# Optimization experiments

Hardware: AMD Instinct MI355X
Metric: run time of the kernel (lower is better)

Reference implementation:

```python
import jax, jax.numpy as jnp
import numpy as np

IMG_H, IMG_W = 256, 704  # full image shape (img_metas['img_shape'])
EPS = 1e-5
B, N_CAM, D_REF, C_CH = 1, 6, 1, 256
HF, WF = 32, 88
DD = 64
BEV_H = BEV_W = 128
Q = BEV_H * BEV_W


def inverse_sigmoid(x, eps=1e-5):
    x = jnp.clip(x, 0.0, 1.0)
    return jnp.log(jnp.clip(x, eps) / jnp.clip(1.0 - x, eps))


def grid_sample_2d(feat, grid):
    # feat [N,C,H,W], grid [N,Hg,Wg,2] (x,y in [-1,1]); bilinear, zeros padding, align_corners=False
    Nn, C, H, W = feat.shape
    x = (grid[..., 0] + 1.0) * 0.5 * W - 0.5
    y = (grid[..., 1] + 1.0) * 0.5 * H - 0.5
    x0 = jnp.floor(x)
    y0 = jnp.floor(y)
    wx = x - x0
    wy = y - y0
    x0 = x0.astype(jnp.int32)
    y0 = y0.astype(jnp.int32)

    def gather(ix, iy):
        valid = (ix >= 0) & (ix < W) & (iy >= 0) & (iy < H)
        ixc = jnp.clip(ix, 0, W - 1)
        iyc = jnp.clip(iy, 0, H - 1)
        v = jax.vmap(lambda f, jx, jy: f[:, jy, jx])(feat, ixc, iyc)  # [N,C,Hg,Wg]
        return v * valid[:, None].astype(feat.dtype)

    return (gather(x0, y0) * ((1 - wx) * (1 - wy))[:, None]
            + gather(x0 + 1, y0) * (wx * (1 - wy))[:, None]
            + gather(x0, y0 + 1) * ((1 - wx) * wy)[:, None]
            + gather(x0 + 1, y0 + 1) * (wx * wy)[:, None])


def grid_sample_3d(vol, grid):
    # vol [N,C,D,H,W], grid [N,Dg,Hg,Wg,3] (x,y,z); trilinear, zeros padding, align_corners=False
    Nn, C, D, H, W = vol.shape
    x = (grid[..., 0] + 1.0) * 0.5 * W - 0.5
    y = (grid[..., 1] + 1.0) * 0.5 * H - 0.5
    z = (grid[..., 2] + 1.0) * 0.5 * D - 0.5
    x0 = jnp.floor(x); y0 = jnp.floor(y); z0 = jnp.floor(z)
    wx = x - x0; wy = y - y0; wz = z - z0
    x0 = x0.astype(jnp.int32); y0 = y0.astype(jnp.int32); z0 = z0.astype(jnp.int32)

    def gather(ix, iy, iz):
        valid = (ix >= 0) & (ix < W) & (iy >= 0) & (iy < H) & (iz >= 0) & (iz < D)
        ixc = jnp.clip(ix, 0, W - 1)
        iyc = jnp.clip(iy, 0, H - 1)
        izc = jnp.clip(iz, 0, D - 1)
        v = jax.vmap(lambda f, jx, jy, jz: f[:, jz, jy, jx])(vol, ixc, iyc, izc)
        return v * valid[:, None].astype(vol.dtype)

    return (gather(x0, y0, z0) * ((1 - wx) * (1 - wy) * (1 - wz))[:, None]
            + gather(x0 + 1, y0, z0) * (wx * (1 - wy) * (1 - wz))[:, None]
            + gather(x0, y0 + 1, z0) * ((1 - wx) * wy * (1 - wz))[:, None]
            + gather(x0 + 1, y0 + 1, z0) * (wx * wy * (1 - wz))[:, None]
            + gather(x0, y0, z0 + 1) * ((1 - wx) * (1 - wy) * wz)[:, None]
            + gather(x0 + 1, y0, z0 + 1) * (wx * (1 - wy) * wz)[:, None]
            + gather(x0, y0 + 1, z0 + 1) * ((1 - wx) * wy * wz)[:, None]
            + gather(x0 + 1, y0 + 1, z0 + 1) * (wx * wy * wz)[:, None])


def setup_inputs() -> dict:
    key = jax.random.key(0)
    ks = jax.random.split(key, 12)
    feat = jax.random.normal(ks[0], (B * N_CAM, C_CH, HF, WF), jnp.float32)
    bev_queries = jax.random.normal(ks[1], (B, Q, C_CH), jnp.float32)
    bev_pos = jax.random.normal(ks[2], (B, Q, C_CH), jnp.float32)
    reference_points = jax.random.uniform(ks[3], (B, D_REF, Q, 3), jnp.float32)
    pc_range = jnp.array([-51.2, -51.2, -5.0, 51.2, 51.2, 3.0], jnp.float32)
    # semi-realistic lidar->image projection matrices: intrinsics * axis-swap * yaw per camera
    f, cx, cy = 500.0, IMG_W / 2.0, IMG_H / 2.0
    K = np.array([[f, 0, cx, 0], [0, f, cy, 0], [0, 0, 1, 0], [0, 0, 0, 1]], np.float32)
    A = np.array([[0, -1, 0, 0], [0, 0, -1, 0], [1, 0, 0, 0], [0, 0, 0, 1]], np.float32)
    mats = []
    for i in range(N_CAM):
        th = 2.0 * np.pi * i / N_CAM
        c, s = np.cos(th), np.sin(th)
        R = np.array([[c, s, 0, 0], [-s, c, 0, 0], [0, 0, 1, 0], [0, 0, 0, 1]], np.float32)
        mats.append(K @ A @ R)
    lidar_to_img = jnp.asarray(np.stack(mats))[None]  # [1,N,4,4]
    depth_prob = jax.random.uniform(ks[4], (B * N_CAM, DD, HF, WF), jnp.float32)
    sc = 0.02
    return {
        'feat': feat, 'bev_queries': bev_queries, 'bev_pos': bev_pos,
        'reference_points': reference_points, 'pc_range': pc_range,
        'lidar_to_img': lidar_to_img, 'depth_prob': depth_prob,
        'w_pos': jax.random.normal(ks[5], (C_CH, 1), jnp.float32) * sc,
        'b_pos': jnp.zeros((1,), jnp.float32),
        'w_img': jax.random.normal(ks[6], (C_CH, N_CAM * 2), jnp.float32) * sc,
        'b_img': jnp.zeros((N_CAM * 2,), jnp.float32),
        'w_att': jax.random.normal(ks[7], (C_CH, N_CAM), jnp.float32) * sc,
        'b_att': jnp.zeros((N_CAM,), jnp.float32),
        'conv_w': jax.random.normal(ks[8], (C_CH, C_CH, 3, 3), jnp.float32) * sc,
        'conv_b': jnp.zeros((C_CH,), jnp.float32),
        'bn_gamma': jnp.ones((C_CH,), jnp.float32),
        'bn_beta': jnp.zeros((C_CH,), jnp.float32),
        'bn_mean': jnp.zeros((C_CH,), jnp.float32),
        'bn_var': jnp.ones((C_CH,), jnp.float32),
        'se_w': jax.random.normal(ks[9], (C_CH, C_CH), jnp.float32) * sc,
        'se_b': jnp.zeros((C_CH,), jnp.float32),
        'cbam_w': jax.random.normal(ks[10], (1, 2, 7, 7), jnp.float32) * 0.05,
        'cbam_b': jnp.zeros((1,), jnp.float32),
        'bev_h': BEV_H, 'bev_w': BEV_W,
    }


def reference(feat, bev_queries, bev_pos, reference_points, pc_range, lidar_to_img, depth_prob,
              w_pos, b_pos, w_img, b_img, w_att, b_att, conv_w, conv_b,
              bn_gamma, bn_beta, bn_mean, bn_var, se_w, se_b, cbam_w, cbam_b, bev_h, bev_w):
    Bq, Qn = bev_queries.shape[:2]
    D = reference_points.shape[1]
    N = lidar_to_img.shape[1]
    BN, C, Hf, Wf = feat.shape
    q = bev_queries + bev_pos
    pos_offset = q @ w_pos + b_pos  # [B,Q,1] (only_use_height)
    z = jax.nn.sigmoid(inverse_sigmoid(reference_points[..., 2:3]) + pos_offset[:, None])
    rp = jnp.concatenate([reference_points[..., :2], z], axis=-1)  # [B,D,Q,3]
    attn = (q @ w_att + b_att).reshape(Bq, 1, Qn, N, 1)
    img_off = q @ w_img + b_img  # [B,Q,2N]
    # unnormalize to lidar coords; apply_3d_transformation == identity (no aug)
    pts = rp * (pc_range[3:] - pc_range[:3]) + pc_range[:3]
    pts4 = jnp.concatenate([pts, jnp.ones_like(pts[..., :1])], axis=-1)  # [B,D,Q,4]
    cam = jnp.einsum('bnij,bdqj->dbnqi', lidar_to_img, pts4)  # [D,B,N,Q,4]
    ref_depth = cam[..., 2:3]
    mask = ref_depth > EPS
    xy = cam[..., :2] / jnp.maximum(cam[..., 2:3], EPS)
    xy = xy / jnp.array([IMG_W, IMG_H], dtype=xy.dtype)
    xy = (xy - 0.5) * 2.0
    mask = mask & (xy[..., 0:1] > -1.0) & (xy[..., 0:1] < 1.0) & (xy[..., 1:2] > -1.0) & (xy[..., 1:2] < 1.0)
    Dd = depth_prob.shape[1]
    ref_depth = (ref_depth / Dd - 0.5) * 2.0
    mask = mask & (ref_depth > -1.0) & (ref_depth < 1.0)
    bev_mask = jnp.transpose(mask, (1, 4, 3, 2, 0)).astype(feat.dtype)  # [B,1,Q,N,D]
    off = img_off.reshape(Bq, Qn, N, 2).transpose(0, 2, 1, 3)[None] / jnp.array([Wf, Hf], dtype=feat.dtype)
    xy = xy + off  # [D,B,N,Q,2]
    grid = xy.transpose(1, 2, 3, 0, 4).reshape(BN, Qn, D, 2)
    sampled = grid_sample_2d(feat, grid).reshape(Bq, N, C, Qn, D).transpose(0, 2, 3, 1, 4)  # [B,C,Q,N,D]
    grid3 = jnp.concatenate([xy, ref_depth], axis=-1).transpose(1, 2, 3, 0, 4).reshape(BN, 1, Qn, D, 3)
    dp = grid_sample_3d(depth_prob[:, None], grid3).reshape(Bq, N, 1, Qn, D).transpose(0, 2, 3, 1, 4)
    bev_mask = jnp.nan_to_num(dp) * bev_mask
    w = jax.nn.sigmoid(attn) * jnp.nan_to_num(bev_mask)
    agg = (jnp.nan_to_num(sampled) * w)[..., 0].sum(-1)  # [B,C,Q] (D==1)
    x = agg.reshape(Bq, C, bev_h, bev_w)
    dn = ('NCHW', 'OIHW', 'NCHW')
    x = jax.lax.conv_general_dilated(x, conv_w, (1, 1), ((1, 1), (1, 1)), dimension_numbers=dn) + conv_b[None, :, None, None]
    x = (x - bn_mean[None, :, None, None]) * (bn_gamma / jnp.sqrt(bn_var + 1e-5))[None, :, None, None] + bn_beta[None, :, None, None]
    x = jax.nn.relu(x)
    s = x.mean(axis=(2, 3))  # SE: global avg pool + 1x1 conv + sigmoid
    x = x * jax.nn.sigmoid(s @ se_w.T + se_b)[:, :, None, None]
    a = jnp.concatenate([x.max(axis=1, keepdims=True), x.mean(axis=1, keepdims=True)], axis=1)  # CBAM spatial
    a = jax.lax.conv_general_dilated(a, cbam_w, (1, 1), ((3, 3), (3, 3)), dimension_numbers=dn) + cbam_b[None, :, None, None]
    x = x * jax.nn.sigmoid(a)
    out = x.reshape(Bq, C, bev_h * bev_w).transpose(0, 2, 1)
    return out, rp
```

## Files before the change

kernel.cpp:

```cpp
#include <hip/hip_runtime.h>
#include <math.h>

#define QN   16384
#define CCH  256
#define NCAM 6
#define HFD  32
#define WFD  88
#define DDD  64
#define BEVH 128
#define BEVW 128
#define IMGW 704.0f
#define IMGH 256.0f
#define EPSV 1e-5f

typedef __attribute__((ext_vector_type(8))) short bf8_t;
typedef __attribute__((ext_vector_type(8))) unsigned short us8;
typedef __attribute__((ext_vector_type(4))) unsigned short us4;
typedef __attribute__((ext_vector_type(4))) float f4_t;

__device__ __forceinline__ float sigmoidf_(float x){ return 1.0f/(1.0f+__expf(-x)); }

__device__ __forceinline__ unsigned short f2bf(float f){
    unsigned int b = __float_as_uint(f);
    b += 0x7FFFu + ((b >> 16) & 1u);
    return (unsigned short)(b >> 16);
}
__device__ __forceinline__ float bf2f(unsigned short u){
    return __uint_as_float(((unsigned int)u) << 16);
}

__global__ __launch_bounds__(256) void k_prep(const float* __restrict__ feat, unsigned short* __restrict__ feat_tH,
                                              const float* __restrict__ cw, unsigned short* __restrict__ wtH,
                                              const float* __restrict__ se_w, float* __restrict__ se_wT,
                                              float* __restrict__ ssum){
    int b = blockIdx.x;
    if (b < 4224){
        __shared__ float tile[32][33];
        int n   = b / 704;
        int rem = b - n*704;
        int cb  = (rem / 88) * 32;
        int pb  = (rem % 88) * 32;
        int tx = threadIdx.x & 31, ty = threadIdx.x >> 5;
        for (int r = ty; r < 32; r += 8)
            tile[r][tx] = feat[(size_t)(n*256 + cb + r)*2816 + pb + tx];
        __syncthreads();
        for (int r = ty; r < 32; r += 8)
            feat_tH[(size_t)(n*2816 + pb + r)*256 + cb + tx] = f2bf(tile[tx][r]);
    } else if (b < 6528){
        int b2 = b - 4224;
        if (b2 == 0) ssum[threadIdx.x] = 0.f;
        int idx = b2*256 + threadIdx.x;
        int ci = idx & 255;
        int co = (idx >> 8) & 255;
        int kk = idx >> 16;
        int kh = kk/3, kw = kk - kh*3;
        int chunk = ci >> 6, ciin = ci & 63;
        size_t dst = ((((size_t)(kh*4 + chunk)*3 + kw)*256 + co) << 6) + ciin;
        wtH[dst] = f2bf(cw[(size_t)(co*256 + ci)*9 + kk]);
    } else {
        __shared__ float tile[32][33];
        int tb = b - 6528;
        int rb_ = (tb >> 3) * 32;
        int cb_ = (tb & 7) * 32;
        int tx = threadIdx.x & 31, ty = threadIdx.x >> 5;
        for (int r = ty; r < 32; r += 8)
            tile[r][tx] = se_w[(size_t)(rb_ + r)*256 + cb_ + tx];
        __syncthreads();
        for (int r = ty; r < 32; r += 8)
            se_wT[(size_t)(cb_ + r)*256 + rb_ + tx] = tile[tx][r];
    }
}

__global__ __launch_bounds__(256) void k_proj(
    const float* __restrict__ bq, const float* __restrict__ bpos,
    const float* __restrict__ refp,
    const float* __restrict__ w_pos, const float* __restrict__ b_pos,
    const float* __restrict__ w_img, const float* __restrict__ w_att,
    float* __restrict__ Sg, float* __restrict__ out_rp)
{
    __shared__ float wlf[19][260];
    __shared__ unsigned short Aq[64][264];
    __shared__ float sl[64][20];
    int tid = threadIdx.x;
    int lane = tid & 63, wid = tid >> 6;
    int l15 = lane & 15, quad = lane >> 4;
    int q0 = blockIdx.x * 64;

    wlf[0][tid] = w_pos[tid];
    #pragma unroll
    for (int r = 0; r < 6; r++){
        int idx = r*256 + tid;
        int c = idx / 6, j = idx - 6*c;
        wlf[1 + j][c] = w_att[idx];
    }
    #pragma unroll
    for (int r = 0; r < 12; r++){
        int idx = r*256 + tid;
        int c = idx / 12, j = idx - 12*c;
        wlf[7 + j][c] = w_img[idx];
    }
    #pragma unroll
    for (int r = 0; r < 16; r++){
        int row = r*4 + wid;
        int cc  = lane * 4;
        float4 a = *(const float4*)(bq   + (size_t)(q0+row)*CCH + cc);
        float4 b = *(const float4*)(bpos + (size_t)(q0+row)*CCH + cc);
        us4 o;
        o.x = f2bf(a.x+b.x); o.y = f2bf(a.y+b.y); o.z = f2bf(a.z+b.z); o.w = f2bf(a.w+b.w);
        *(us4*)&Aq[row][cc] = o;
    }
    __syncthreads();

    f4_t acc0 = (f4_t){0.f,0.f,0.f,0.f};
    f4_t acc1 = (f4_t){0.f,0.f,0.f,0.f};
    #pragma unroll
    for (int kc = 0; kc < 8; kc++){
        bf8_t af = *(bf8_t*)&Aq[wid*16 + l15][kc*32 + quad*8];
        bf8_t b0, b1;
        {
            const float* wr = &wlf[l15][kc*32 + quad*8];
            float4 w0 = *(const float4*)wr;
            float4 w1 = *(const float4*)(wr + 4);
            b0[0]=(short)f2bf(w0.x); b0[1]=(short)f2bf(w0.y); b0[2]=(short)f2bf(w0.z); b0[3]=(short)f2bf(w0.w);
            b0[4]=(short)f2bf(w1.x); b0[5]=(short)f2bf(w1.y); b0[6]=(short)f2bf(w1.z); b0[7]=(short)f2bf(w1.w);
        }
        if (l15 < 3){
            const float* wr = &wlf[16 + l15][kc*32 + quad*8];
            float4 w0 = *(const float4*)wr;
            float4 w1 = *(const float4*)(wr + 4);
            b1[0]=(short)f2bf(w0.x); b1[1]=(short)f2bf(w0.y); b1[2]=(short)f2bf(w0.z); b1[3]=(short)f2bf(w0.w);
            b1[4]=(short)f2bf(w1.x); b1[5]=(short)f2bf(w1.y); b1[6]=(short)f2bf(w1.z); b1[7]=(short)f2bf(w1.w);
        } else {
            b1 = (bf8_t){0,0,0,0,0,0,0,0};
        }
        acc0 = __builtin_amdgcn_mfma_f32_16x16x32_bf16(af, b0, acc0, 0, 0, 0);
        acc1 = __builtin_amdgcn_mfma_f32_16x16x32_bf16(af, b1, acc1, 0, 0, 0);
    }
    #pragma unroll
    for (int r = 0; r < 4; r++){
        int qq = wid*16 + quad*4 + r;
        sl[qq][l15] = acc0[r];
        if (l15 < 3) sl[qq][16 + l15] = acc1[r];
    }
    __syncthreads();

    if (tid < 64){
        int q = q0 + tid;
        float pos_off = sl[tid][0] + b_pos[0];
        float rx = refp[q*3+0], ry = refp[q*3+1], rz = refp[q*3+2];
        float zc_ = fminf(fmaxf(rz, 0.f), 1.f);
        float inv = logf(fmaxf(zc_, EPSV) / fmaxf(1.f - zc_, EPSV));
        float znew = sigmoidf_(inv + pos_off);
        out_rp[q*3+0] = rx; out_rp[q*3+1] = ry; out_rp[q*3+2] = znew;
        sl[tid][19] = znew;
    }
    __syncthreads();

    for (int i = tid; i < 64*20; i += 256)
        Sg[(size_t)q0*20 + i] = ((const float*)sl)[i];
}

__global__ __launch_bounds__(256) void k_geomagg(
    const float* __restrict__ refp, const float* __restrict__ pcr,
    const float* __restrict__ l2i, const float* __restrict__ dpr,
    const float* __restrict__ b_img, const float* __restrict__ b_att,
    const float* __restrict__ Sg, const unsigned short* __restrict__ feat_tH,
    unsigned short* __restrict__ aggH)
{
    __shared__ float sgl[8][20];
    __shared__ int   so_l[192];
    __shared__ float sw_l[192];
    int q0 = blockIdx.x * 8;
    int tid = threadIdx.x;
    int wid = tid >> 6, lane = tid & 63;

    if (tid < 160) ((float*)sgl)[tid] = Sg[(size_t)q0*20 + tid];
    __syncthreads();

    {
        int sub = lane >> 5;
        int n   = lane & 31;
        if (n < NCAM){
            int ql = wid*2 + sub;
            int q  = q0 + ql;
            float att  = sgl[ql][1+n] + b_att[n];
            float offx = (sgl[ql][7+2*n] + b_img[2*n])   / (float)WFD;
            float offy = (sgl[ql][8+2*n] + b_img[2*n+1]) / (float)HFD;
            float znew = sgl[ql][19];
            float rx = refp[q*3+0], ry = refp[q*3+1];
            float lo0=pcr[0], lo1=pcr[1], lo2=pcr[2];
            float hi0=pcr[3], hi1=pcr[4], hi2=pcr[5];
            float px = rx*(hi0-lo0)+lo0, py = ry*(hi1-lo1)+lo1, pz = znew*(hi2-lo2)+lo2;
            const float* M = l2i + n*16;
            float cx = M[0]*px + M[1]*py + M[2]*pz  + M[3];
            float cy = M[4]*px + M[5]*py + M[6]*pz  + M[7];
            float cz = M[8]*px + M[9]*py + M[10]*pz + M[11];
            bool m = cz > EPSV;
            float zdiv = fmaxf(cz, EPSV);
            float u = (cx/zdiv)/IMGW; u = (u - 0.5f)*2.f;
            float v = (cy/zdiv)/IMGH; v = (v - 0.5f)*2.f;
            m = m && (u > -1.f) && (u < 1.f) && (v > -1.f) && (v < 1.f);
            float rdn = (cz/(float)DDD - 0.5f)*2.f;
            m = m && (rdn > -1.f) && (rdn < 1.f);

            int base = ql*24 + n*4;
            float wq = 0.f, xs = 0.f, ys = 0.f;
            if (m){
                float u2 = u + offx, v2 = v + offy;
                xs = (u2 + 1.f)*0.5f*WFD - 0.5f;
                ys = (v2 + 1.f)*0.5f*HFD - 0.5f;
                float zs = (rdn + 1.f)*0.5f*DDD - 0.5f;
                float fx = floorf(xs), fy = floorf(ys), fz = floorf(zs);
                int x0=(int)fx, y0=(int)fy, z0=(int)fz;
                float wx = xs-fx, wy = ys-fy, wz = zs-fz;
                float dp = 0.f;
                const float* vol = dpr + (size_t)n*DDD*HFD*WFD;
                #pragma unroll
                for (int dz=0; dz<2; dz++)
                #pragma unroll
                for (int dy=0; dy<2; dy++)
                #pragma unroll
                for (int dx=0; dx<2; dx++){
                    int ix=x0+dx, iy=y0+dy, iz=z0+dz;
                    if (ix>=0 && ix<WFD && iy>=0 && iy<HFD && iz>=0 && iz<DDD){
                        float ww = (dx?wx:1.f-wx)*(dy?wy:1.f-wy)*(dz?wz:1.f-wz);
                        dp += ww * vol[(size_t)(iz*HFD+iy)*WFD + ix];
                    }
                }
                wq = sigmoidf_(att) * dp;
            }
            if (m && wq != 0.f){
                float fx = floorf(xs), fy = floorf(ys);
                int x0=(int)fx, y0=(int)fy;
                float wx = xs-fx, wy = ys-fy;
                float cwv[4] = {(1.f-wx)*(1.f-wy), wx*(1.f-wy), (1.f-wx)*wy, wx*wy};
                int xi[4] = {x0, x0+1, x0, x0+1};
                int yi[4] = {y0, y0, y0+1, y0+1};
                #pragma unroll
                for (int k=0;k<4;k++){
                    bool ok = (xi[k]>=0 && xi[k]<WFD && yi[k]>=0 && yi[k]<HFD);
                    so_l[base+k] = ok ? ((n*HFD + yi[k])*WFD + xi[k]) : 0;
                    sw_l[base+k] = ok ? wq*cwv[k] : 0.f;
                }
            } else {
                #pragma unroll
                for (int k=0;k<4;k++){ so_l[base+k] = 0; sw_l[base+k] = 0.f; }
            }
        }
    }
    __syncthreads();

    {
        int half = lane >> 5, li = lane & 31;
        int c8 = li * 8;
        int ql = wid*2 + half;
        float a[8] = {0.f,0.f,0.f,0.f,0.f,0.f,0.f,0.f};
        #pragma unroll
        for (int k=0;k<24;k++){
            float w = sw_l[ql*24+k];
            us8 v = *(const us8*)(feat_tH + (size_t)so_l[ql*24+k]*CCH + c8);
            #pragma unroll
            for (int j=0;j<8;j++) a[j] += w * bf2f((unsigned short)v[j]);
        }
        us8 o;
        #pragma unroll
        for (int j=0;j<8;j++) o[j] = f2bf(a[j]);
        *(us8*)(aggH + (size_t)(q0+ql)*CCH + c8) = o;
    }
}

__global__ __launch_bounds__(256, 2) void k_conv2(const unsigned short* __restrict__ aggH,
    const unsigned short* __restrict__ wtH, const float* __restrict__ conv_b,
    const float* __restrict__ bn_g, const float* __restrict__ bn_b,
    const float* __restrict__ bn_m, const float* __restrict__ bn_v,
    float* __restrict__ xN, float* __restrict__ ssum)
{
    __shared__ unsigned short Al[130][72];
    __shared__ unsigned short Bl[3][128][72];
    __shared__ float sacc[128];

    int h   = blockIdx.x;
    int co0 = blockIdx.y * 128;
    int tid  = threadIdx.x;
    int lane = tid & 63, wid = tid >> 6;
    int m_q = (wid & 1) * 64;
    int n_q = (wid >> 1) * 64;
    int l15 = lane & 15, quad = lane >> 4;

    f4_t acc[4][4];
    #pragma unroll
    for (int i=0;i<4;i++)
    #pragma unroll
    for (int j=0;j<4;j++) acc[i][j] = (f4_t){0.f,0.f,0.f,0.f};

    int arow = tid >> 1;
    int aseg = (tid & 1) * 32;

    if (tid < 16){
        int r = (tid >> 3) ? 129 : 0;
        int sg = (tid & 7) * 8;
        *(us8*)&Al[r][sg] = (us8){0,0,0,0,0,0,0,0};
    }
    if (tid < 128) sacc[tid] = 0.f;

    us8 ra[4], rb[3][4];
    const us8 z8 = (us8){0,0,0,0,0,0,0,0};

    #define LOADSTAGE(s) { \
        int kh_ = (s) >> 2; \
        int ph_ = h + kh_ - 1; \
        if (ph_ >= 0 && ph_ < BEVH){ \
            const unsigned short* ap_ = aggH + ((size_t)(ph_*BEVW + arow)*CCH + (((s) & 3) << 6) + aseg); \
            ra[0] = *(const us8*)ap_;        ra[1] = *(const us8*)(ap_ + 8); \
            ra[2] = *(const us8*)(ap_ + 16); ra[3] = *(const us8*)(ap_ + 24); \
        } else { ra[0]=z8; ra[1]=z8; ra[2]=z8; ra[3]=z8; } \
        const unsigned short* bp_ = wtH + (size_t)(s)*49152 + (size_t)co0*64; \
        _Pragma("unroll") \
        for (int kw_=0; kw_<3; kw_++){ \
            _Pragma("unroll") \
            for (int j_=0; j_<4; j_++) \
                rb[kw_][j_] = *(const us8*)(bp_ + kw_*16384 + (j_*256 + tid)*8); \
        } \
    }

    LOADSTAGE(0);
    for (int s=0; s<12; s++){
        __syncthreads();
        *(us8*)&Al[arow+1][aseg]      = ra[0];
        *(us8*)&Al[arow+1][aseg+8]    = ra[1];
        *(us8*)&Al[arow+1][aseg+16]   = ra[2];
        *(us8*)&Al[arow+1][aseg+24]   = ra[3];
        {
            int bco = tid >> 3;
            int ciin = (tid & 7) * 8;
            #pragma unroll
            for (int kw_=0; kw_<3; kw_++){
                #pragma unroll
                for (int j_=0; j_<4; j_++)
                    *(us8*)&Bl[kw_][j_*32 + bco][ciin] = rb[kw_][j_];
            }
        }
        __syncthreads();
        if (s < 11) LOADSTAGE(s+1);
        #pragma unroll
        for (int ks=0; ks<2; ks++){
            #pragma unroll
            for (int kw=0; kw<3; kw++){
                bf8_t af[4], bfr[4];
                #pragma unroll
                for (int i=0;i<4;i++) af[i]  = *(bf8_t*)&Al[m_q + i*16 + l15 + kw][ks*32 + quad*8];
                #pragma unroll
                for (int j=0;j<4;j++) bfr[j] = *(bf8_t*)&Bl[kw][n_q + j*16 + l15][ks*32 + quad*8];
                #pragma unroll
                for (int i=0;i<4;i++)
                #pragma unroll
                for (int j=0;j<4;j++)
                    acc[i][j] = __builtin_amdgcn_mfma_f32_16x16x32_bf16(af[i], bfr[j], acc[i][j], 0, 0, 0);
            }
        }
    }
    #undef LOADSTAGE

    #pragma unroll
    for (int j=0;j<4;j++){
        int col = n_q + j*16 + l15;
        int co = co0 + col;
        float sc = bn_g[co] * rsqrtf(bn_v[co] + 1e-5f);
        float sh = bn_b[co] - bn_m[co]*sc;
        float cb = conv_b[co];
        float part = 0.f;
        #pragma unroll
        for (int i=0;i<4;i++){
            #pragma unroll
            for (int r=0;r<4;r++){
                int m = m_q + i*16 + quad*4 + r;
                int p = h*BEVW + m;
                float y = fmaxf((acc[i][j][r] + cb)*sc + sh, 0.f);
                xN[(size_t)p*CCH + co] = y;
                part += y;
            }
        }
        atomicAdd(&sacc[col], part);
    }
    __syncthreads();
    if (tid < 128) atomicAdd(&ssum[co0 + tid], sacc[tid]);
}

__global__ __launch_bounds__(256) void k_maps2(const float* __restrict__ xN,
    const float* __restrict__ ssum, const float* __restrict__ se_wT, const float* __restrict__ se_b,
    float* __restrict__ scale_g, float* __restrict__ amax, float* __restrict__ amean)
{
    __shared__ float smv[256];
    __shared__ float scl[256];
    int t = threadIdx.x;
    smv[t] = ssum[t] * (1.f/16384.f);
    __syncthreads();
    float a0=0.f, a1=0.f, a2=0.f, a3=0.f;
    for (int k=0; k<256; k+=4){
        a0 += smv[k]   * se_wT[(size_t)(k  )*256 + t];
        a1 += smv[k+1] * se_wT[(size_t)(k+1)*256 + t];
        a2 += smv[k+2] * se_wT[(size_t)(k+2)*256 + t];
        a3 += smv[k+3] * se_wT[(size_t)(k+3)*256 + t];
    }
    float sv = sigmoidf_(se_b[t] + ((a0+a1)+(a2+a3)));
    scl[t] = sv;
    if (blockIdx.x == 0) scale_g[t] = sv;
    __syncthreads();

    int wid = t >> 6, lane = t & 63;
    int p0 = blockIdx.x * 64;
    float4 sc = *(const float4*)&scl[lane*4];
    for (int i=0; i<16; i++){
        int p = p0 + i*4 + wid;
        float4 v = *(const float4*)&xN[(size_t)p*CCH + lane*4];
        float a = v.x*sc.x, b = v.y*sc.y, c = v.z*sc.z, d = v.w*sc.w;
        float mx = fmaxf(fmaxf(a,b), fmaxf(c,d));
        float sm = a+b+c+d;
        #pragma unroll
        for (int off=1; off<64; off<<=1){
            mx = fmaxf(mx, __shfl_xor(mx, off, 64));
            sm += __shfl_xor(sm, off, 64);
        }
        if (lane == 0){ amax[p] = mx; amean[p] = sm*(1.f/256.f); }
    }
}

__global__ __launch_bounds__(256) void k_final2(const float* __restrict__ xN,
    const float* __restrict__ scale_g, const float* __restrict__ amax, const float* __restrict__ amean,
    const float* __restrict__ cw, const float* __restrict__ cb, float* __restrict__ out)
{
    __shared__ float am2[7][128];
    __shared__ float av2[7][128];
    __shared__ float wcb[98];
    __shared__ float scl[256];
    __shared__ float amap_l[64];

    int b = blockIdx.x;
    int h  = b >> 1;
    int w0 = (b & 1) * 64;
    int t = threadIdx.x;

    scl[t] = scale_g[t];
    if (t < 98) wcb[t] = cw[t];
    for (int idx = t; idx < 896; idx += 256){
        int r = idx >> 7, c = idx & 127;
        int ph = h + r - 3;
        bool ok = (ph >= 0 && ph < BEVH);
        am2[r][c] = ok ? amax[ph*BEVW + c] : 0.f;
        av2[r][c] = ok ? amean[ph*BEVW + c] : 0.f;
    }
    __syncthreads();

    if (t < 64){
        int px = w0 + t;
        float acc = cb[0];
        #pragma unroll
        for (int kh=0; kh<7; kh++){
            #pragma unroll
            for (int kw=0; kw<7; kw++){
                int pw = px + kw - 3;
                if (pw >= 0 && pw < BEVW)
                    acc += am2[kh][pw]*wcb[kh*7+kw] + av2[kh][pw]*wcb[49 + kh*7+kw];
            }
        }
        amap_l[t] = sigmoidf_(acc);
    }
    __syncthreads();

    int lane = t & 63, sub = t >> 6;
    int c4 = lane * 4;
    float4 sc = *(const float4*)&scl[c4];
    for (int i=0; i<16; i++){
        int pxl = sub*16 + i;
        int p = h*BEVW + w0 + pxl;
        float am = amap_l[pxl];
        float4 v = *(const float4*)&xN[(size_t)p*CCH + c4];
        float4 o;
        o.x = v.x*sc.x*am; o.y = v.y*sc.y*am; o.z = v.z*sc.z*am; o.w = v.w*sc.w*am;
        *(float4*)&out[(size_t)p*CCH + c4] = o;
    }
}

extern "C" void kernel_launch(void* const* d_in, const int* in_sizes, int n_in,
                              void* d_out, int out_size, void* d_ws, size_t ws_size,
                              hipStream_t stream) {
    const float* feat   = (const float*)d_in[0];
    const float* bq     = (const float*)d_in[1];
    const float* bpos   = (const float*)d_in[2];
    const float* refp   = (const float*)d_in[3];
    const float* pcr    = (const float*)d_in[4];
    const float* l2i    = (const float*)d_in[5];
    const float* dpr    = (const float*)d_in[6];
    const float* w_pos  = (const float*)d_in[7];
    const float* b_pos  = (const float*)d_in[8];
    const float* w_img  = (const float*)d_in[9];
    const float* b_img  = (const float*)d_in[10];
    const float* w_att  = (const float*)d_in[11];
    const float* b_att  = (const float*)d_in[12];
    const float* conv_w = (const float*)d_in[13];
    const float* conv_b = (const float*)d_in[14];
    const float* bn_g   = (const float*)d_in[15];
    const float* bn_b   = (const float*)d_in[16];
    const float* bn_m   = (const float*)d_in[17];
    const float* bn_v   = (const float*)d_in[18];
    const float* se_w   = (const float*)d_in[19];
    const float* se_b   = (const float*)d_in[20];
    const float* cbw    = (const float*)d_in[21];
    const float* cbb    = (const float*)d_in[22];
    float* out = (float*)d_out;

    float* ws = (float*)d_ws;
    size_t o = 0;
    unsigned short* feat_tH = (unsigned short*)(ws + o); o += (size_t)6*2816*128;
    unsigned short* wtH  = (unsigned short*)(ws + o); o += (size_t)9*256*128;
    unsigned short* aggH = (unsigned short*)(ws + o); o += (size_t)QN*128;
    float* xN      = ws + o;  o += (size_t)QN*256;
    float* se_wT   = ws + o;  o += (size_t)256*256;
    float* Sg      = ws + o;  o += (size_t)QN*20;
    float* ssum    = ws + o;  o += 256;
    float* scale_g = ws + o;  o += 256;
    float* amax    = ws + o;  o += QN;
    float* amean   = ws + o;  o += QN;

    k_prep<<<6592, 256, 0, stream>>>(feat, feat_tH, conv_w, wtH, se_w, se_wT, ssum);
    k_proj<<<256, 256, 0, stream>>>(bq, bpos, refp, w_pos, b_pos, w_img, w_att,
                                    Sg, out + (size_t)QN*256);
    k_geomagg<<<2048, 256, 0, stream>>>(refp, pcr, l2i, dpr, b_img, b_att,
                                        Sg, feat_tH, aggH);
    k_conv2<<<dim3(128,2), 256, 0, stream>>>(aggH, wtH, conv_b, bn_g, bn_b, bn_m, bn_v, xN, ssum);
    k_maps2<<<256, 256, 0, stream>>>(xN, ssum, se_wT, se_b, scale_g, amax, amean);
    k_final2<<<256, 256, 0, stream>>>(xN, scale_g, amax, amean, cbw, cbb, out);
}
```

Measured before the change: 221.2 us.

## Split conv K dimension across two blocks and add separate activation reduce kernel

The 3x3 conv kernel now splits its 12 K-stages between two z-blocks, doubling the grid from 256 to 512 blocks so more CUs are occupied. Each block writes raw fp32 partial sums to its own buffer. A new k_act kernel adds the two partials, applies bias, batchnorm and ReLU, and accumulates the SE channel sums. The LDS row padding also changes from 72 to 76 to alter the bank mapping. The cost is two extra 16 MB fp32 buffers, one written and later read, plus an additional kernel launch.

After: 247.8 us. +12.0%, slower.

```diff
diff --git a/kernel.cpp b/kernel.cpp
--- a/kernel.cpp
+++ b/kernel.cpp
@@ -270,17 +270,15 @@
 }
 
 __global__ __launch_bounds__(256, 2) void k_conv2(const unsigned short* __restrict__ aggH,
-    const unsigned short* __restrict__ wtH, const float* __restrict__ conv_b,
-    const float* __restrict__ bn_g, const float* __restrict__ bn_b,
-    const float* __restrict__ bn_m, const float* __restrict__ bn_v,
-    float* __restrict__ xN, float* __restrict__ ssum)
+    const unsigned short* __restrict__ wtH,
+    float* __restrict__ xNa, float* __restrict__ xNb)
 {
-    __shared__ unsigned short Al[130][72];
-    __shared__ unsigned short Bl[3][128][72];
-    __shared__ float sacc[128];
+    __shared__ unsigned short Al[130][76];
+    __shared__ unsigned short Bl[3][128][76];
 
     int h   = blockIdx.x;
     int co0 = blockIdx.y * 128;
+    int z   = blockIdx.z;
     int tid  = threadIdx.x;
     int lane = tid & 63, wid = tid >> 6;
     int m_q = (wid & 1) * 64;
@@ -301,20 +299,20 @@
         int sg = (tid & 7) * 8;
         *(us8*)&Al[r][sg] = (us8){0,0,0,0,0,0,0,0};
     }
-    if (tid < 128) sacc[tid] = 0.f;
 
     us8 ra[4], rb[3][4];
     const us8 z8 = (us8){0,0,0,0,0,0,0,0};
 
-    #define LOADSTAGE(s) { \
-        int kh_ = (s) >> 2; \
+    #define SFULL(sp) ((((sp) >> 1) << 2) + (z << 1) + ((sp) & 1))
+    #define LOADSTAGE(sf) { \
+        int kh_ = (sf) >> 2; \
         int ph_ = h + kh_ - 1; \
         if (ph_ >= 0 && ph_ < BEVH){ \
-            const unsigned short* ap_ = aggH + ((size_t)(ph_*BEVW + arow)*CCH + (((s) & 3) << 6) + aseg); \
+            const unsigned short* ap_ = aggH + ((size_t)(ph_*BEVW + arow)*CCH + (((sf) & 3) << 6) + aseg); \
             ra[0] = *(const us8*)ap_;        ra[1] = *(const us8*)(ap_ + 8); \
             ra[2] = *(const us8*)(ap_ + 16); ra[3] = *(const us8*)(ap_ + 24); \
         } else { ra[0]=z8; ra[1]=z8; ra[2]=z8; ra[3]=z8; } \
-        const unsigned short* bp_ = wtH + (size_t)(s)*49152 + (size_t)co0*64; \
+        const unsigned short* bp_ = wtH + (size_t)(sf)*49152 + (size_t)co0*64; \
         _Pragma("unroll") \
         for (int kw_=0; kw_<3; kw_++){ \
             _Pragma("unroll") \
@@ -323,8 +321,8 @@
         } \
     }
 
-    LOADSTAGE(0);
-    for (int s=0; s<12; s++){
+    LOADSTAGE(SFULL(0));
+    for (int sp=0; sp<6; sp++){
         __syncthreads();
         *(us8*)&Al[arow+1][aseg]      = ra[0];
         *(us8*)&Al[arow+1][aseg+8]    = ra[1];
@@ -341,7 +339,7 @@
             }
         }
         __syncthreads();
-        if (s < 11) LOADSTAGE(s+1);
+        if (sp < 5) LOADSTAGE(SFULL(sp+1));
         #pragma unroll
         for (int ks=0; ks<2; ks++){
             #pragma unroll
@@ -360,30 +358,68 @@
         }
     }
     #undef LOADSTAGE
-
+    #undef SFULL
+
+    float* __restrict__ xO = z ? xNb : xNa;
     #pragma unroll
     for (int j=0;j<4;j++){
-        int col = n_q + j*16 + l15;
-        int co = co0 + col;
-        float sc = bn_g[co] * rsqrtf(bn_v[co] + 1e-5f);
-        float sh = bn_b[co] - bn_m[co]*sc;
-        float cb = conv_b[co];
-        float part = 0.f;
+        int co = co0 + n_q + j*16 + l15;
         #pragma unroll
         for (int i=0;i<4;i++){
             #pragma unroll
             for (int r=0;r<4;r++){
                 int m = m_q + i*16 + quad*4 + r;
-                int p = h*BEVW + m;
-                float y = fmaxf((acc[i][j][r] + cb)*sc + sh, 0.f);
-                xN[(size_t)p*CCH + co] = y;
-                part += y;
+                xO[(size_t)(h*BEVW + m)*CCH + co] = acc[i][j][r];
             }
         }
-        atomicAdd(&sacc[col], part);
-    }
-    __syncthreads();
-    if (tid < 128) atomicAdd(&ssum[co0 + tid], sacc[tid]);
+    }
+}
+
+__global__ __launch_bounds__(256) void k_act(const float* __restrict__ xNa, const float* __restrict__ xNb,
+    const float* __restrict__ conv_b, const float* __restrict__ bn_g, const float* __restrict__ bn_b,
+    const float* __restrict__ bn_m, const float* __restrict__ bn_v,
+    float* __restrict__ xN, float* __restrict__ ssum)
+{
+    __shared__ float red[4][256];
+    int t = threadIdx.x, lane = t & 63, wid = t >> 6;
+    int c4 = lane * 4;
+    float4 g  = *(const float4*)&bn_g[c4];
+    float4 vv = *(const float4*)&bn_v[c4];
+    float4 mm = *(const float4*)&bn_m[c4];
+    float4 bb = *(const float4*)&bn_b[c4];
+    float4 cb = *(const float4*)&conv_b[c4];
+    float4 sc, sh;
+    sc.x = g.x*rsqrtf(vv.x+1e-5f); sc.y = g.y*rsqrtf(vv.y+1e-5f);
+    sc.z = g.z*rsqrtf(vv.z+1e-5f); sc.w = g.w*rsqrtf(vv.w+1e-5f);
+    sh.x = bb.x - mm.x*sc.x; sh.y = bb.y - mm.y*sc.y;
+    sh.z = bb.z - mm.z*sc.z; sh.w = bb.w - mm.w*sc.w;
+
+    float4 sum = {0.f,0.f,0.f,0.f};
+    int p0 = blockIdx.x * 64;
+    for (int i=0;i<16;i++){
+        int p = p0 + i*4 + wid;
+        float4 a = *(const float4*)&xNa[(size_t)p*CCH + c4];
+        float4 b = *(const float4*)&xNb[(size_t)p*CCH + c4];
+        float4 y;
+        y.x = fmaxf((a.x+b.x+cb.x)*sc.x+sh.x, 0.f);
+        y.y = fmaxf((a.y+b.y+cb.y)*sc.y+sh.y, 0.f);
+        y.z = fmaxf((a.z+b.z+cb.z)*sc.z+sh.z, 0.f);
+        y.w = fmaxf((a.w+b.w+cb.w)*sc.w+sh.w, 0.f);
+        *(float4*)&xN[(size_t)p*CCH + c4] = y;
+        sum.x += y.x; sum.y += y.y; sum.z += y.z; sum.w += y.w;
+    }
+    *(float4*)&red[wid][c4] = sum;
+    __syncthreads();
+    if (wid == 0){
+        float4 s0 = *(const float4*)&red[0][c4];
+        float4 s1 = *(const float4*)&red[1][c4];
+        float4 s2 = *(const float4*)&red[2][c4];
+        float4 s3 = *(const float4*)&red[3][c4];
+        atomicAdd(&ssum[c4+0], (s0.x+s1.x)+(s2.x+s3.x));
+        atomicAdd(&ssum[c4+1], (s0.y+s1.y)+(s2.y+s3.y));
+        atomicAdd(&ssum[c4+2], (s0.z+s1.z)+(s2.z+s3.z));
+        atomicAdd(&ssum[c4+3], (s0.w+s1.w)+(s2.w+s3.w));
+    }
 }
 
 __global__ __launch_bounds__(256) void k_maps2(const float* __restrict__ xN,
@@ -515,6 +551,8 @@
     unsigned short* wtH  = (unsigned short*)(ws + o); o += (size_t)9*256*128;
     unsigned short* aggH = (unsigned short*)(ws + o); o += (size_t)QN*128;
     float* xN      = ws + o;  o += (size_t)QN*256;
+    float* xNa     = ws + o;  o += (size_t)QN*256;
+    float* xNb     = ws + o;  o += (size_t)QN*256;
     float* se_wT   = ws + o;  o += (size_t)256*256;
     float* Sg      = ws + o;  o += (size_t)QN*20;
     float* ssum    = ws + o;  o += 256;
@@ -527,7 +565,8 @@
                                     Sg, out + (size_t)QN*256);
     k_geomagg<<<2048, 256, 0, stream>>>(refp, pcr, l2i, dpr, b_img, b_att,
                                         Sg, feat_tH, aggH);
-    k_conv2<<<dim3(128,2), 256, 0, stream>>>(aggH, wtH, conv_b, bn_g, bn_b, bn_m, bn_v, xN, ssum);
+    k_conv2<<<dim3(128,2,2), 256, 0, stream>>>(aggH, wtH, xNa, xNb);
+    k_act<<<256, 256, 0, stream>>>(xNa, xNb, conv_b, bn_g, bn_b, bn_m, bn_v, xN, ssum);
     k_maps2<<<256, 256, 0, stream>>>(xN, ssum, se_wT, se_b, scale_g, amax, amean);
     k_final2<<<256, 256, 0, stream>>>(xN, scale_g, amax, amean, cbw, cbb, out);
 }
```
